# Performance work log

Measured on AMD Instinct MI355X. Metric: run time of the kernel, lower is better.

## Reference

```python
import jax, jax.numpy as jnp
import numpy as np

B, T, D, F = 4, 2048, 4096, 16384
EQN = 'btd,df->btf'  # fixed einsum equation (contracting axis = D, axis 0 of kernel)


def setup_inputs() -> dict:
    key = jax.random.key(0)
    k1, k2, k3 = jax.random.split(key, 3)
    x = jax.random.normal(k1, (B, T, D), dtype=jnp.float32)
    # int8-quantized kernel weights stored as integers
    kernel = jax.random.randint(k2, (D, F), -127, 128, dtype=jnp.int32).astype(jnp.int8)
    # per-output-channel dequant scale, shape (1, F) per deduce_scale_shape
    scale = jax.random.uniform(k3, (1, F), dtype=jnp.float32, minval=0.5, maxval=1.5)
    return {"x": x, "kernel": kernel, "scale": scale}


def reference(x, kernel, scale):
    # dequantize: cast int kernel to activation dtype, divide by per-channel scale
    k = kernel.astype(x.dtype) / scale  # [D, F]
    return jnp.einsum(EQN, x, k)  # [B, T, F]
```

## Files before the change

kernel.cpp:

```cpp
#include <hip/hip_runtime.h>


namespace {

constexpr int MD = 8192;
constexpr int ND = 16384;
constexpr int KD = 4096;
constexpr int NT = KD / 64;

typedef float fl4 __attribute__((ext_vector_type(4)));
typedef unsigned int u32x4 __attribute__((ext_vector_type(4)));
typedef int i32x4 __attribute__((ext_vector_type(4)));

__device__ __forceinline__ unsigned int pack4(fl4 v, float sc) {
  int q0 = __float2int_rn(v.x * sc);
  int q1 = __float2int_rn(v.y * sc);
  int q2 = __float2int_rn(v.z * sc);
  int q3 = __float2int_rn(v.w * sc);
  return (q0 & 0xFF) | ((q1 & 0xFF) << 8) | ((q2 & 0xFF) << 16) |
         ((q3 & 0xFF) << 24);
}

__global__ __launch_bounds__(256) void quant_x_kernel(
    const float* __restrict__ x, signed char* __restrict__ xq,
    float* __restrict__ xs) {
  const int row = blockIdx.x;
  const int t   = threadIdx.x;
  const float* xr = x + (size_t)row * KD + t * 16;
  fl4 v0 = *(const fl4*)(xr);
  fl4 v1 = *(const fl4*)(xr + 4);
  fl4 v2 = *(const fl4*)(xr + 8);
  fl4 v3 = *(const fl4*)(xr + 12);
  float m = 0.f;
  m = fmaxf(m, fmaxf(fmaxf(fabsf(v0.x), fabsf(v0.y)), fmaxf(fabsf(v0.z), fabsf(v0.w))));
  m = fmaxf(m, fmaxf(fmaxf(fabsf(v1.x), fabsf(v1.y)), fmaxf(fabsf(v1.z), fabsf(v1.w))));
  m = fmaxf(m, fmaxf(fmaxf(fabsf(v2.x), fabsf(v2.y)), fmaxf(fabsf(v2.z), fabsf(v2.w))));
  m = fmaxf(m, fmaxf(fmaxf(fabsf(v3.x), fabsf(v3.y)), fmaxf(fabsf(v3.z), fabsf(v3.w))));
#pragma unroll
  for (int off = 32; off; off >>= 1) m = fmaxf(m, __shfl_xor(m, off));
  __shared__ float red[4];
  if ((t & 63) == 0) red[t >> 6] = m;
  __syncthreads();
  m = fmaxf(fmaxf(red[0], red[1]), fmaxf(red[2], red[3]));
  const float sc = (m > 0.f) ? 127.0f / m : 0.f;
  if (t == 0) xs[row] = (m > 0.f) ? m / 127.0f : 0.f;
  u32x4 o;
  o.x = pack4(v0, sc);
  o.y = pack4(v1, sc);
  o.z = pack4(v2, sc);
  o.w = pack4(v3, sc);
  *(u32x4*)(xq + (size_t)row * KD + t * 16) = o;
}

__global__ __launch_bounds__(256) void transpose_w_kernel(
    const int* __restrict__ W, signed char* __restrict__ WT) {
  constexpr int KC = 64;
  const int nb = blockIdx.x & 63;
  const int kb = blockIdx.x >> 6;
  const int n  = nb * 256 + threadIdx.x;
  const int k0 = kb * KC;
  const int* src = W + (size_t)k0 * ND + n;
  unsigned int buf[16];
#pragma unroll
  for (int i = 0; i < KC; i += 4) {
    unsigned int b0 = (unsigned)src[(size_t)(i + 0) * ND] & 0xFF;
    unsigned int b1 = (unsigned)src[(size_t)(i + 1) * ND] & 0xFF;
    unsigned int b2 = (unsigned)src[(size_t)(i + 2) * ND] & 0xFF;
    unsigned int b3 = (unsigned)src[(size_t)(i + 3) * ND] & 0xFF;
    buf[i >> 2] = b0 | (b1 << 8) | (b2 << 16) | (b3 << 24);
  }
  u32x4* dst = (u32x4*)(WT + (size_t)n * KD + k0);
#pragma unroll
  for (int j = 0; j < 4; ++j) {
    u32x4 o;
    o.x = buf[4 * j + 0];
    o.y = buf[4 * j + 1];
    o.z = buf[4 * j + 2];
    o.w = buf[4 * j + 3];
    dst[j] = o;
  }
}


#define GLL16(g, l)                                                  \
  __builtin_amdgcn_global_load_lds(                                  \
      (const __attribute__((address_space(1))) void*)(g),            \
      (__attribute__((address_space(3))) void*)(l), 16, 0, 0)

#define BARRIER()    __builtin_amdgcn_s_barrier()
#define WAITL(N)     asm volatile("s_waitcnt lgkmcnt(" #N ")")
#define WAITV(N)     asm volatile("s_waitcnt vmcnt(" #N ")")
#define SCHED()      __builtin_amdgcn_sched_barrier(0)
#define PRIO1()      __builtin_amdgcn_s_setprio(1)
#define PRIO0()      __builtin_amdgcn_s_setprio(0)

__global__ __launch_bounds__(512, 4) void gemm_kernel(
    const signed char* __restrict__ Aq8,
    const signed char* __restrict__ Bq8,
    const float* __restrict__ xs,
    const float* __restrict__ scale,
    float* __restrict__ C) {
  __shared__ __align__(16) char Asm[2][16384];
  __shared__ __align__(16) char Bsm[2][8192];

  const int tid  = threadIdx.x;
  const int lane = tid & 63;
  const int w    = tid >> 6;
  const int wm   = w >> 1;
  const int wn   = w & 1;

  const int bid = blockIdx.x;
  const int xcd = bid & 7;
  const int pos = bid >> 3;
  const int tm  = (xcd << 2) | (pos & 3);
  const int tn  = pos >> 2;
  const size_t brow = (size_t)tm * 256;
  const size_t bcol = (size_t)tn * 128;

  const int srow  = tid >> 2;
  const int sgran = (tid & 3) ^ ((tid >> 3) & 3);
  const signed char* Ag = Aq8 + (brow + srow) * (size_t)KD + sgran * 16;
  const signed char* Bg = Bq8 + (bcol + srow) * (size_t)KD + sgran * 16;

  const int r15  = lane & 15;
  const int kcsw = (((lane >> 4) ^ ((r15 >> 1) & 3)) << 4);

  i32x4 acc[4][4];
#pragma unroll
  for (int i = 0; i < 4; ++i)
#pragma unroll
    for (int j = 0; j < 4; ++j) acc[i][j] = (i32x4){0, 0, 0, 0};

  {
    GLL16(Ag,                        &Asm[0][0] + w * 1024);
    GLL16(Ag + (size_t)128 * KD,     &Asm[0][8192] + w * 1024);
    GLL16(Bg,                        &Bsm[0][0] + w * 1024);
    GLL16(Ag + 64,                   &Asm[1][0] + w * 1024);
    GLL16(Ag + (size_t)128 * KD + 64, &Asm[1][8192] + w * 1024);
    GLL16(Bg + 64,                   &Bsm[1][0] + w * 1024);
  }
  SCHED();
  WAITV(3);
  SCHED();
  BARRIER();
  SCHED();

  i32x4 a[4], b[4];
  {
    const char* Ab = &Asm[0][0] + (wm * 64 + r15) * 64 + kcsw;
#pragma unroll
    for (int mi = 0; mi < 4; ++mi) a[mi] = *(const i32x4*)(Ab + mi * 1024);
  }
  SCHED();

#pragma unroll 2
  for (int it = 0; it < NT; ++it) {
    const int h = it & 1;
    const char* Bb  = &Bsm[h][0] + (wn * 64 + r15) * 64 + kcsw;
    const char* AbN = &Asm[h ^ 1][0] + (wm * 64 + r15) * 64 + kcsw;
    const size_t kb2 = (size_t)((it + 2) & (NT - 1)) * 64;

#pragma unroll
    for (int ni = 0; ni < 4; ++ni) b[ni] = *(const i32x4*)(Bb + ni * 1024);
    SCHED();
    WAITL(2);
    SCHED();
    PRIO1();
#pragma unroll
    for (int mi = 0; mi < 4; ++mi)
#pragma unroll
      for (int ni = 0; ni < 2; ++ni)
        acc[mi][ni] = __builtin_amdgcn_mfma_i32_16x16x64_i8(
            a[mi], b[ni], acc[mi][ni], 0, 0, 0);
    PRIO0();
    SCHED();
    WAITL(0);
    SCHED();
    PRIO1();
#pragma unroll
    for (int mi = 0; mi < 2; ++mi)
#pragma unroll
      for (int ni = 2; ni < 4; ++ni)
        acc[mi][ni] = __builtin_amdgcn_mfma_i32_16x16x64_i8(
            a[mi], b[ni], acc[mi][ni], 0, 0, 0);
    PRIO0();
    SCHED();
    WAITV(0);
    SCHED();
    BARRIER();
    SCHED();
    GLL16(Ag + kb2,                        &Asm[h][0] + w * 1024);
    GLL16(Ag + (size_t)128 * KD + kb2,     &Asm[h][8192] + w * 1024);
    GLL16(Bg + kb2,                        &Bsm[h][0] + w * 1024);
    SCHED();
    PRIO1();
#pragma unroll
    for (int mi = 2; mi < 4; ++mi)
#pragma unroll
      for (int ni = 2; ni < 4; ++ni)
        acc[mi][ni] = __builtin_amdgcn_mfma_i32_16x16x64_i8(
            a[mi], b[ni], acc[mi][ni], 0, 0, 0);
    PRIO0();
    SCHED();
#pragma unroll
    for (int mi = 0; mi < 4; ++mi) a[mi] = *(const i32x4*)(AbN + mi * 1024);
    SCHED();
  }

  const int r4 = (lane >> 4) << 2;
  float sxv[4][4];
#pragma unroll
  for (int mi = 0; mi < 4; ++mi)
#pragma unroll
    for (int r = 0; r < 4; ++r)
      sxv[mi][r] = xs[brow + wm * 64 + mi * 16 + r4 + r];
#pragma unroll
  for (int ni = 0; ni < 4; ++ni) {
    const size_t col = bcol + wn * 64 + ni * 16 + r15;
    const float inv = 1.0f / scale[col];
#pragma unroll
    for (int mi = 0; mi < 4; ++mi) {
      float* cp = C + (brow + wm * 64 + mi * 16 + r4) * (size_t)ND + col;
#pragma unroll
      for (int r = 0; r < 4; ++r)
        cp[(size_t)r * ND] = (float)acc[mi][ni][r] * sxv[mi][r] * inv;
    }
  }
}

}

extern "C" void kernel_launch(void* const* d_in, const int* in_sizes, int n_in,
                              void* d_out, int out_size, void* d_ws,
                              size_t ws_size, hipStream_t stream) {
  const float* x     = (const float*)d_in[0];
  const int*   W     = (const int*)d_in[1];
  const float* scale = (const float*)d_in[2];
  float*       out   = (float*)d_out;

  signed char* xq = (signed char*)d_ws;
  signed char* wq = (signed char*)d_ws + (size_t)32 * 1024 * 1024;
  float*       xs = (float*)((char*)d_ws + (size_t)96 * 1024 * 1024);

  quant_x_kernel<<<8192, 256, 0, stream>>>(x, xq, xs);
  transpose_w_kernel<<<4096, 256, 0, stream>>>(W, wq);
  gemm_kernel<<<4096, 512, 0, stream>>>(xq, wq, xs, scale, out);
}
```

Baseline: 745.7 us.

## Shrink GEMM tile to 128x128 with 256 threads and register double-buffered fragments

Halves the block tile from 256x128 to 128x128 and uses 4 waves (256 threads) instead of 8, launching twice as many blocks. The main loop is restructured into a ping-pong register scheme: after the barrier it loads the next A/B fragments from LDS into a second register set, issues the global-to-LDS prefetch, then runs all 16 MFMAs on the current fragments. The old split-phase MFMA schedule with partial lgkmcnt waits is replaced by a single wait. The smaller tile lowers arithmetic intensity and increases global traffic per FLOP, in exchange for more blocks, more occupancy and simpler overlap.

```diff
diff --git a/kernel.cpp b/kernel.cpp
--- a/kernel.cpp
+++ b/kernel.cpp
@@ -88,19 +88,19 @@
       (__attribute__((address_space(3))) void*)(l), 16, 0, 0)
 
 #define BARRIER()    __builtin_amdgcn_s_barrier()
-#define WAITL(N)     asm volatile("s_waitcnt lgkmcnt(" #N ")")
+#define WAITL0()     asm volatile("s_waitcnt lgkmcnt(0)")
 #define WAITV(N)     asm volatile("s_waitcnt vmcnt(" #N ")")
 #define SCHED()      __builtin_amdgcn_sched_barrier(0)
 #define PRIO1()      __builtin_amdgcn_s_setprio(1)
 #define PRIO0()      __builtin_amdgcn_s_setprio(0)
 
-__global__ __launch_bounds__(512, 4) void gemm_kernel(
+__global__ __launch_bounds__(256, 3) void gemm_kernel(
     const signed char* __restrict__ Aq8,
     const signed char* __restrict__ Bq8,
     const float* __restrict__ xs,
     const float* __restrict__ scale,
     float* __restrict__ C) {
-  __shared__ __align__(16) char Asm[2][16384];
+  __shared__ __align__(16) char Asm[2][8192];
   __shared__ __align__(16) char Bsm[2][8192];
 
   const int tid  = threadIdx.x;
@@ -112,9 +112,9 @@
   const int bid = blockIdx.x;
   const int xcd = bid & 7;
   const int pos = bid >> 3;
-  const int tm  = (xcd << 2) | (pos & 3);
-  const int tn  = pos >> 2;
-  const size_t brow = (size_t)tm * 256;
+  const int tm  = (xcd << 3) | (pos & 7);
+  const int tn  = pos >> 3;
+  const size_t brow = (size_t)tm * 128;
   const size_t bcol = (size_t)tn * 128;
 
   const int srow  = tid >> 2;
@@ -124,6 +124,8 @@
 
   const int r15  = lane & 15;
   const int kcsw = (((lane >> 4) ^ ((r15 >> 1) & 3)) << 4);
+  const int aoff = (wm * 64 + r15) * 64 + kcsw;
+  const int boff = (wn * 64 + r15) * 64 + kcsw;
 
   i32x4 acc[4][4];
 #pragma unroll
@@ -131,81 +133,62 @@
 #pragma unroll
     for (int j = 0; j < 4; ++j) acc[i][j] = (i32x4){0, 0, 0, 0};
 
-  {
-    GLL16(Ag,                        &Asm[0][0] + w * 1024);
-    GLL16(Ag + (size_t)128 * KD,     &Asm[0][8192] + w * 1024);
-    GLL16(Bg,                        &Bsm[0][0] + w * 1024);
-    GLL16(Ag + 64,                   &Asm[1][0] + w * 1024);
-    GLL16(Ag + (size_t)128 * KD + 64, &Asm[1][8192] + w * 1024);
-    GLL16(Bg + 64,                   &Bsm[1][0] + w * 1024);
-  }
-  SCHED();
-  WAITV(3);
+  GLL16(Ag,                        &Asm[0][0] + w * 1024);
+  GLL16(Ag + (size_t)64 * KD,      &Asm[0][4096] + w * 1024);
+  GLL16(Bg,                        &Bsm[0][0] + w * 1024);
+  GLL16(Bg + (size_t)64 * KD,      &Bsm[0][4096] + w * 1024);
+  GLL16(Ag + 64,                   &Asm[1][0] + w * 1024);
+  GLL16(Ag + (size_t)64 * KD + 64, &Asm[1][4096] + w * 1024);
+  GLL16(Bg + 64,                   &Bsm[1][0] + w * 1024);
+  GLL16(Bg + (size_t)64 * KD + 64, &Bsm[1][4096] + w * 1024);
+  SCHED();
+  WAITV(4);
   SCHED();
   BARRIER();
   SCHED();
 
-  i32x4 a[4], b[4];
-  {
-    const char* Ab = &Asm[0][0] + (wm * 64 + r15) * 64 + kcsw;
-#pragma unroll
-    for (int mi = 0; mi < 4; ++mi) a[mi] = *(const i32x4*)(Ab + mi * 1024);
-  }
-  SCHED();
-
-#pragma unroll 2
-  for (int it = 0; it < NT; ++it) {
-    const int h = it & 1;
-    const char* Bb  = &Bsm[h][0] + (wn * 64 + r15) * 64 + kcsw;
-    const char* AbN = &Asm[h ^ 1][0] + (wm * 64 + r15) * 64 + kcsw;
-    const size_t kb2 = (size_t)((it + 2) & (NT - 1)) * 64;
-
-#pragma unroll
-    for (int ni = 0; ni < 4; ++ni) b[ni] = *(const i32x4*)(Bb + ni * 1024);
-    SCHED();
-    WAITL(2);
-    SCHED();
-    PRIO1();
-#pragma unroll
-    for (int mi = 0; mi < 4; ++mi)
-#pragma unroll
-      for (int ni = 0; ni < 2; ++ni)
-        acc[mi][ni] = __builtin_amdgcn_mfma_i32_16x16x64_i8(
-            a[mi], b[ni], acc[mi][ni], 0, 0, 0);
-    PRIO0();
-    SCHED();
-    WAITL(0);
-    SCHED();
-    PRIO1();
-#pragma unroll
-    for (int mi = 0; mi < 2; ++mi)
-#pragma unroll
-      for (int ni = 2; ni < 4; ++ni)
-        acc[mi][ni] = __builtin_amdgcn_mfma_i32_16x16x64_i8(
-            a[mi], b[ni], acc[mi][ni], 0, 0, 0);
-    PRIO0();
-    SCHED();
-    WAITV(0);
-    SCHED();
-    BARRIER();
-    SCHED();
-    GLL16(Ag + kb2,                        &Asm[h][0] + w * 1024);
-    GLL16(Ag + (size_t)128 * KD + kb2,     &Asm[h][8192] + w * 1024);
-    GLL16(Bg + kb2,                        &Bsm[h][0] + w * 1024);
-    SCHED();
-    PRIO1();
-#pragma unroll
-    for (int mi = 2; mi < 4; ++mi)
-#pragma unroll
-      for (int ni = 2; ni < 4; ++ni)
-        acc[mi][ni] = __builtin_amdgcn_mfma_i32_16x16x64_i8(
-            a[mi], b[ni], acc[mi][ni], 0, 0, 0);
-    PRIO0();
-    SCHED();
-#pragma unroll
-    for (int mi = 0; mi < 4; ++mi) a[mi] = *(const i32x4*)(AbN + mi * 1024);
-    SCHED();
-  }
+  i32x4 a0[4], b0[4], a1[4], b1[4];
+#pragma unroll
+  for (int mi = 0; mi < 4; ++mi)
+    a0[mi] = *(const i32x4*)(&Asm[0][0] + aoff + mi * 1024);
+#pragma unroll
+  for (int ni = 0; ni < 4; ++ni)
+    b0[ni] = *(const i32x4*)(&Bsm[0][0] + boff + ni * 1024);
+  SCHED();
+
+#define BODY(T, H, CA, CB, NA, NB)                                            \
+  {                                                                           \
+    const size_t kb2 = (size_t)(((T) + 2) & (NT - 1)) * 64;                   \
+    WAITL0();     \
+    SCHED();                                                                  \
+    WAITV(0);          \
+    SCHED();                                                                  \
+    BARRIER();        \
+    SCHED();                                                                  \
+    _Pragma("unroll") for (int mi = 0; mi < 4; ++mi)                          \
+        NA[mi] = *(const i32x4*)(&Asm[(H) ^ 1][0] + aoff + mi * 1024);        \
+    _Pragma("unroll") for (int ni = 0; ni < 4; ++ni)                          \
+        NB[ni] = *(const i32x4*)(&Bsm[(H) ^ 1][0] + boff + ni * 1024);        \
+    SCHED();                                                                  \
+    GLL16(Ag + kb2,                   &Asm[H][0] + w * 1024);                 \
+    GLL16(Ag + (size_t)64 * KD + kb2, &Asm[H][4096] + w * 1024);              \
+    GLL16(Bg + kb2,                   &Bsm[H][0] + w * 1024);                 \
+    GLL16(Bg + (size_t)64 * KD + kb2, &Bsm[H][4096] + w * 1024);              \
+    SCHED();                                                                  \
+    PRIO1();                                                                  \
+    _Pragma("unroll") for (int mi = 0; mi < 4; ++mi)                          \
+    _Pragma("unroll") for (int ni = 0; ni < 4; ++ni)                          \
+        acc[mi][ni] = __builtin_amdgcn_mfma_i32_16x16x64_i8(                  \
+            CA[mi], CB[ni], acc[mi][ni], 0, 0, 0);                            \
+    PRIO0();                                                                  \
+    SCHED();                                                                  \
+  }
+
+  for (int it = 0; it < NT; it += 2) {
+    BODY(it,     0, a0, b0, a1, b1);
+    BODY(it + 1, 1, a1, b1, a0, b0);
+  }
+#undef BODY
 
   const int r4 = (lane >> 4) << 2;
   float sxv[4][4];
@@ -244,5 +227,5 @@
 
   quant_x_kernel<<<8192, 256, 0, stream>>>(x, xq, xs);
   transpose_w_kernel<<<4096, 256, 0, stream>>>(W, wq);
-  gemm_kernel<<<4096, 512, 0, stream>>>(xq, wq, xs, scale, out);
-}
+  gemm_kernel<<<8192, 256, 0, stream>>>(xq, wq, xs, scale, out);
+}
```

After: 830.9 us. 1.11x slower.
